# Optimization experiments

Hardware: AMD Instinct MI355X
Metric: run time of the kernel (lower is better)

The kernel has to match this reference:

```python
import jax, jax.numpy as jnp
import numpy as np

EPS_W = 1e-9


def area2d(a, b, c):
    # signed parallelogram area; a/b/c are [..., >=2] points
    return (b[..., 0] - a[..., 0]) * (c[..., 1] - a[..., 1]) - (b[..., 1] - a[..., 1]) * (c[..., 0] - a[..., 0])


def lookup_table(size):
    # square table of 2d points (x, y) in [-1, 1], matching torch meshgrid('ij') + rot90
    lin = jnp.linspace(-1.0, 1.0, size, dtype=jnp.float32)
    xx, yy = jnp.meshgrid(lin, lin, indexing='ij')
    t = jnp.stack([xx, yy], axis=-1)
    return jnp.rot90(t, 1, axes=(0, 1))  # [S,S,2]


def grid_sample_bilinear(img, grid):
    # img [C,H,W]; grid [...,2] with (x,y) in [-1,1]; bilinear, zero padding, align_corners=True
    C, H, W = img.shape
    x, y = grid[..., 0], grid[..., 1]
    ix = (x + 1.0) * (W - 1) * 0.5
    iy = (y + 1.0) * (H - 1) * 0.5
    ix0 = jnp.floor(ix)
    iy0 = jnp.floor(iy)
    ix1 = ix0 + 1.0
    iy1 = iy0 + 1.0
    wx1 = ix - ix0
    wx0 = 1.0 - wx1
    wy1 = iy - iy0
    wy0 = 1.0 - wy1

    def tap(iyf, ixf):
        inb = (ixf >= 0) & (ixf <= W - 1) & (iyf >= 0) & (iyf <= H - 1)
        ii = jnp.clip(ixf, 0, W - 1).astype(jnp.int32)
        jj = jnp.clip(iyf, 0, H - 1).astype(jnp.int32)
        return img[:, jj, ii] * inb.astype(img.dtype)  # [C, ...]

    return (tap(iy0, ix0) * (wy0 * wx0) + tap(iy0, ix1) * (wy0 * wx1)
            + tap(iy1, ix0) * (wy1 * wx0) + tap(iy1, ix1) * (wy1 * wx1))


def _render(vertices, uv, uvmap, faces, uvfaces, size):
    pts = lookup_table(size)              # [S,S,2]
    uvn = uv * 2.0 - 1.0                  # uv scaled to [-1,1] as in __init__
    tris = vertices[faces]                # [K,3,3]
    uvt = uvn[uvfaces]                    # [K,3,2]

    # backface cull mask (z-component of cross(v1-v0, v2-v0) > 0)
    e1 = tris[:, 1] - tris[:, 0]
    e2 = tris[:, 2] - tris[:, 0]
    normal_z = e1[:, 0] * e2[:, 1] - e1[:, 1] * e2[:, 0]
    valid = normal_z > 0

    zinit = jnp.min(vertices, axis=0)[-1]
    result0 = jnp.zeros((4, size, size), jnp.float32)
    zbuf0 = jnp.full((size, size), zinit, dtype=jnp.float32)

    def step(carry, xs):
        result, zbuf = carry
        tri, uvtri, ok = xs               # tri [3,3], uvtri [3,2], ok scalar bool
        tri2d = tri[:, :2]
        w = area2d(tri2d[0], tri2d[1], tri2d[2])
        # sub areas against every pixel (dense equivalent of AABB + inside masks)
        pAB = area2d(tri2d[1], pts, tri2d[0])   # [S,S]
        pCB = area2d(tri2d[2], pts, tri2d[1])
        pCA = area2d(tri2d[0], pts, tri2d[2])
        inside = (pAB > 0) & (pCB > 0) & (pCA > 0)
        ws = jnp.where(w >= EPS_W, w, 1.0)      # safe divide; masked out below
        w1 = pCB / ws
        w2 = pCA / ws
        w3 = 1.0 - w1 - w2
        z = w1 * tri[0, 2] + w2 * tri[1, 2] + w3 * tri[2, 2]   # [S,S]
        mask = ok & (w >= EPS_W) & inside & (z >= zbuf)
        # barycentric uv interpolation + bilinear texture lookup
        ptsUV = w1[..., None] * uvtri[0] + w2[..., None] * uvtri[1] + w3[..., None] * uvtri[2]  # [S,S,2]
        rgb = grid_sample_bilinear(uvmap, ptsUV)  # [3,S,S]
        zbuf = jnp.where(mask, z, zbuf)
        rgba = jnp.concatenate([rgb, jnp.ones((1, size, size), result.dtype)], axis=0)
        result = jnp.where(mask[None], rgba, result)
        return (result, zbuf), None

    (result, _), _ = jax.lax.scan(step, (result0, zbuf0), (tris, uvt, valid))
    return result


def setup_inputs() -> dict:
    key = jax.random.key(0)
    k0, k1, k2, k3, k4 = jax.random.split(key, 5)
    V, K, M, T, S = 1500, 1500, 2000, 1024, 512
    vertices = jax.random.normal(k0, (V, 3), dtype=jnp.float32)
    faces = jax.random.randint(k1, (K, 3), 0, V)
    uv = jax.random.uniform(k2, (M, 2), dtype=jnp.float32)
    uvfaces = jax.random.randint(k3, (K, 3), 0, M)
    uvmap = jax.random.normal(k4, (3, T, T), dtype=jnp.float32)
    return {"vertices": vertices, "faces": faces, "uv": uv,
            "uvfaces": uvfaces, "uvmap": uvmap, "size": S}


def reference(vertices, faces, uv, uvfaces, uvmap, size):
    return _render(vertices, uv, uvmap, faces, uvfaces, size)
```

## Files before the change

kernel.cpp:

```cpp
#include <hip/hip_runtime.h>
#include <hip/hip_fp16.h>
#include <cmath>

#pragma clang fp contract(off)

#define MAXK 2048

struct TriUV {
  float u0x, u0y, u1x, u1y;
  float u2x, u2y, pad0, pad1;
};

struct __align__(128) TriRec {
  uint4 ap;
  float4 mt;
  float4 q0;
  float4 q1;
  float4 q2;
  float4 q3;
  float4 pad0, pad1;
};

__device__ __forceinline__ float h2f(unsigned v) {
  __half_raw r; r.x = (unsigned short)v;
  return __half2float(__half(r));
}
__device__ __forceinline__ unsigned f2h(float v) {
  return (unsigned)__half_as_ushort(__float2half(v));
}
__device__ __forceinline__ unsigned pkh(float lo, float hi) {
  return f2h(lo) | (f2h(hi) << 16);
}
__device__ __forceinline__ unsigned fmapu(float f) {
  unsigned b = __float_as_uint(f);
  return (b & 0x80000000u) ? ~b : (b | 0x80000000u);
}
__device__ __forceinline__ float funmap(unsigned m) {
  return __uint_as_float((m & 0x80000000u) ? (m ^ 0x80000000u) : ~m);
}

__device__ __forceinline__ float lin_at(int i, int n) {
#pragma clang fp contract(off)
  if (i == n - 1) return 1.0f;
  float step = (float)i / (float)(n - 1);
  return (-1.0f) * (1.0f - step) + 1.0f * step;
}

__global__ __launch_bounds__(256) void prep_kernel(
    const float* __restrict__ verts, const int* __restrict__ faces,
    const float* __restrict__ uv, const int* __restrict__ uvfaces, int V, int K,
    TriRec* __restrict__ rec, float4* __restrict__ bboxS,
    float4* __restrict__ planeS, TriUV* __restrict__ tuv,
    float* __restrict__ zinit) {
#pragma clang fp contract(off)
  __shared__ float smz[256];
  int tid = (int)threadIdx.x;
  int bid = (int)blockIdx.x;
  if (bid == 0) {
    float m = 3.402823466e38f;
    for (int i = tid; i < V; i += 256) m = fminf(m, verts[3 * i + 2]);
    smz[tid] = m;
    __syncthreads();
    for (int s2 = 128; s2 > 0; s2 >>= 1) {
      if (tid < s2) smz[tid] = fminf(smz[tid], smz[tid + s2]);
      __syncthreads();
    }
    if (tid == 0) *zinit = smz[0];
    return;
  }
  int t = (bid - 1) * 256 + tid;
  if (t >= K) return;
  int i0 = faces[3 * t + 0], i1 = faces[3 * t + 1], i2 = faces[3 * t + 2];
  float t0x = verts[3 * i0 + 0], t0y = verts[3 * i0 + 1], z0 = verts[3 * i0 + 2];
  float t1x = verts[3 * i1 + 0], t1y = verts[3 * i1 + 1], z1 = verts[3 * i1 + 2];
  float t2x = verts[3 * i2 + 0], t2y = verts[3 * i2 + 1], z2 = verts[3 * i2 + 2];
  int j0 = uvfaces[3 * t + 0], j1 = uvfaces[3 * t + 1], j2 = uvfaces[3 * t + 2];
  TriUV u;
  u.u0x = uv[2 * j0 + 0] * 2.0f - 1.0f;
  u.u0y = uv[2 * j0 + 1] * 2.0f - 1.0f;
  u.u1x = uv[2 * j1 + 0] * 2.0f - 1.0f;
  u.u1y = uv[2 * j1 + 1] * 2.0f - 1.0f;
  u.u2x = uv[2 * j2 + 0] * 2.0f - 1.0f;
  u.u2y = uv[2 * j2 + 1] * 2.0f - 1.0f;
  u.pad0 = 0.0f; u.pad1 = 0.0f;
  tuv[t] = u;
  float w = (t1x - t0x) * (t2y - t0y) - (t1y - t0y) * (t2x - t0x);
  if (w < 1e-9f) {
    bboxS[t] = make_float4(3.0e38f, -3.0e38f, 3.0e38f, -3.0e38f);
    return;
  }
  float dAy = t0y - t1y, dAx = t0x - t1x;
  float dBy = t1y - t2y, dBx = t1x - t2x;
  float dCy = t2y - t0y, dCx = t2x - t0x;
  bboxS[t] = make_float4(fminf(fminf(t0x, t1x), t2x),
                         fmaxf(fmaxf(t0x, t1x), t2x),
                         fminf(fminf(t0y, t1y), t2y),
                         fmaxf(fmaxf(t0y, t1y), t2y));
  float fA = t1y * dAx - t1x * dAy;
  float fB = t2y * dBx - t2x * dBy;
  float fC = t0y * dCx - t0x * dCy;
  float sA = fabsf(dAy) + fabsf(dAx) + fabsf(fA);
  float sB = fabsf(dBy) + fabsf(dBx) + fabsf(fB);
  float sC = fabsf(dCy) + fabsf(dCx) + fabsf(fC);
  float M = fmaxf(fmaxf(sA, sB), sC) * 9.766e-4f + 1e-4f;
  TriRec r;
  r.ap = make_uint4(pkh(dAy, dAx), pkh(fA, dBy), pkh(dBx, fB), pkh(dCy, dCx));
  r.mt = make_float4(M, fC, __int_as_float(t), 0.0f);
  r.q0 = make_float4(t1x, t1y, dAy, dAx);
  r.q1 = make_float4(t2x, t2y, dBy, dBx);
  r.q2 = make_float4(t0x, t0y, dCy, dCx);
  r.q3 = make_float4(z0, z1, z2, w);
  r.pad0 = make_float4(0.f, 0.f, 0.f, 0.f);
  r.pad1 = make_float4(0.f, 0.f, 0.f, 0.f);
  rec[t] = r;
  float zmx = fmaxf(fmaxf(z0, z1), z2);
  float gatef = zmx + 1e-3f + 1e-4f / w;
  float gx = (z0 * dBy + z1 * dCy + z2 * dAy) / w;
  float gy = -(z0 * dBx + z1 * dCx + z2 * dAx) / w;
  float cc = (z0 * fB + z1 * fC + z2 * fA) / w;
  float mm = (fabsf(z0 * fB) + fabsf(z1 * fC) + fabsf(z2 * fA) +
              fabsf(z0 * dBy) + fabsf(z1 * dCy) + fabsf(z2 * dAy) +
              fabsf(z0 * dBx) + fabsf(z1 * dCx) + fabsf(z2 * dAx)) *
                 (2e-6f / w) +
             1e-3f + 1e-4f / w + 1e-4f;
  planeS[t] = make_float4(gx, gy, cc + mm, gatef);
}

__global__ __launch_bounds__(1024) void render_kernel(
    const TriRec* __restrict__ rec, const float4* __restrict__ bboxS,
    const float4* __restrict__ planeS, int N, const TriUV* __restrict__ tuv,
    const float* __restrict__ zinitp, const float* __restrict__ uvmap, int T,
    float* __restrict__ out, int S) {
#pragma clang fp contract(off)
  __shared__ uint4 s_g[MAXK];
  __shared__ unsigned long long s_key[256];
  __shared__ unsigned s_zu[256];
  __shared__ unsigned s_hist[256];
  __shared__ int s_cur[256];
  __shared__ unsigned s_wsum[4];

  int tid = (int)threadIdx.x;
  int wv = tid >> 6, ln = tid & 63;
  int s = wv >> 2, q = wv & 3;
  int pix = (q << 6) + ln;
  int tilesX = S >> 4;
  int tileX = (int)blockIdx.x % tilesX;
  int tileY = (int)blockIdx.x / tilesX;
  int j = (tileX << 4) + (pix & 15);
  int i = (tileY << 4) + (pix >> 4);
  float px = lin_at(j, S);
  float py = lin_at(S - 1 - i, S);
  float pxlo = lin_at(tileX << 4, S);
  float pxhi = lin_at((tileX << 4) + 15, S);
  float pylo = lin_at(S - 1 - ((tileY << 4) + 15), S);
  float pyhi = lin_at(S - 1 - (tileY << 4), S);

  float zinit = *zinitp;
  unsigned zinit_m = fmapu(zinit);
  if (tid < 256) {
    s_zu[tid] = zinit_m;
    s_key[tid] = ((unsigned long long)zinit_m << 32);
    s_hist[tid] = 0u;
  }
  volatile unsigned* vzu = s_zu;
  __syncthreads();

  bool kA = false, kB = false;
  int bA = 0, bB = 0;
  unsigned gA = 0, gB = 0;
  {
    int t = tid;
    if (t < N) {
      float4 bb = bboxS[t];
      if (bb.x <= pxhi && bb.y >= pxlo && bb.z <= pyhi && bb.w >= pylo) {
        float4 pl = planeS[t];
        float ub = pl.z + fmaxf(pl.x * pxlo, pl.x * pxhi) +
                   fmaxf(pl.y * pylo, pl.y * pyhi);
        float tg = fminf(pl.w, ub);
        kA = true;
        bA = min(max((int)((4.0f - tg) * 32.0f), 0), 255);
        gA = fmapu(tg);
      }
    }
    t = tid + 1024;
    if (t < N) {
      float4 bb = bboxS[t];
      if (bb.x <= pxhi && bb.y >= pxlo && bb.z <= pyhi && bb.w >= pylo) {
        float4 pl = planeS[t];
        float ub = pl.z + fmaxf(pl.x * pxlo, pl.x * pxhi) +
                   fmaxf(pl.y * pylo, pl.y * pyhi);
        float tg = fminf(pl.w, ub);
        kB = true;
        bB = min(max((int)((4.0f - tg) * 32.0f), 0), 255);
        gB = fmapu(tg);
      }
    }
  }
  if (kA) atomicAdd(&s_hist[bA], 1u);
  if (kB) atomicAdd(&s_hist[bB], 1u);
  __syncthreads();
  unsigned hx = 0, hinc = 0;
  if (tid < 256) {
    hx = s_hist[tid];
    unsigned v = hx;
#pragma unroll
    for (int d = 1; d < 64; d <<= 1) {
      unsigned tv = __shfl_up(v, d, 64);
      if (ln >= d) v += tv;
    }
    if (ln == 63) s_wsum[wv] = v;
    hinc = v;
  }
  __syncthreads();
  if (tid < 256) {
    unsigned add = 0;
    for (int w2 = 0; w2 < wv; ++w2) add += s_wsum[w2];
    hinc += add;
    s_hist[tid] = hinc;
    s_cur[tid] = (int)(hinc - hx);
  }
  __syncthreads();
  int nk = (int)s_hist[255];
  if (kA) {
    int sl = atomicAdd(&s_cur[bA], 1);
    float ef = (bA == 0) ? 3.402823466e38f : (4.0f - (float)bA * 0.03125f);
    s_g[sl] = make_uint4(fmapu(ef), gA, (unsigned)tid, 0u);
  }
  if (kB) {
    int sl = atomicAdd(&s_cur[bB], 1);
    float ef = (bB == 0) ? 3.402823466e38f : (4.0f - (float)bB * 0.03125f);
    s_g[sl] = make_uint4(fmapu(ef), gB, (unsigned)(tid + 1024), 0u);
  }
  __syncthreads();

  for (int a = s; a < nk; a += 4) {
    uint4 g = s_g[a];
    unsigned zb = vzu[pix];
    if (__all(g.x < zb)) break;
    if (g.y >= zb) {
      const TriRec* r = &rec[g.z];
      uint4 ap = r->ap;
      float4 mt = r->mt;
      float M = mt.x, fC = mt.y;
      float aA = fmaf(px, h2f(ap.x & 0xffffu),
                      fmaf(-py, h2f(ap.x >> 16), h2f(ap.y & 0xffffu)));
      float aB = fmaf(px, h2f(ap.y >> 16),
                      fmaf(-py, h2f(ap.z & 0xffffu), h2f(ap.z >> 16)));
      float aC = fmaf(px, h2f(ap.w & 0xffffu),
                      fmaf(-py, h2f(ap.w >> 16), fC));
      if (fminf(fminf(aA, aB), aC) > -M) {
        float4 q0 = r->q0, q1 = r->q1, q2 = r->q2;
        float pAB = (px - q0.x) * q0.z - (py - q0.y) * q0.w;
        float pCB = (px - q1.x) * q1.z - (py - q1.y) * q1.w;
        float pCA = (px - q2.x) * q2.z - (py - q2.y) * q2.w;
        if (pAB > 0.0f && pCB > 0.0f && pCA > 0.0f) {
          float4 q3 = r->q3;
          float w = q3.w;
          float bzf = funmap(vzu[pix]);
          float zs = (pCB * q3.x + pCA * q3.y) + ((w - pCB) - pCA) * q3.z;
          if (w < 1e-3f || zs >= (bzf - 1e-3f) * w) {
            float w1 = pCB / w;
            float w2 = pCA / w;
            float w3 = (1.0f - w1) - w2;
            float z = (w1 * q3.x + w2 * q3.y) + w3 * q3.z;
            int o = __float_as_int(mt.z);
            unsigned zm = fmapu(z);
            unsigned long long key =
                ((unsigned long long)zm << 32) | (unsigned)(o + 1);
            atomicMax(&s_key[pix], key);
            atomicMax(&s_zu[pix], zm);
          }
        }
      }
    }
  }
  __syncthreads();

  if (tid < 256) {
    unsigned long long key = s_key[tid];
    unsigned oP1 = (unsigned)(key & 0xFFFFFFFFULL);
    float o0 = 0.0f, o1 = 0.0f, o2 = 0.0f, o3 = 0.0f;
    if (oP1 != 0) {
      int o = (int)oP1 - 1;
      const TriRec* r = &rec[o];
      float4 q1 = r->q1, q2 = r->q2, q3 = r->q3;
      float pCB = (px - q1.x) * q1.z - (py - q1.y) * q1.w;
      float pCA = (px - q2.x) * q2.z - (py - q2.y) * q2.w;
      float w1 = pCB / q3.w;
      float w2 = pCA / q3.w;
      float w3 = (1.0f - w1) - w2;
      TriUV u = tuv[o];
      float x = (w1 * u.u0x + w2 * u.u1x) + w3 * u.u2x;
      float y = (w1 * u.u0y + w2 * u.u1y) + w3 * u.u2y;
      float WH = (float)(T - 1);
      float fx = ((x + 1.0f) * WH) * 0.5f;
      float fy = ((y + 1.0f) * WH) * 0.5f;
      float ix0 = floorf(fx), iy0 = floorf(fy);
      float ix1 = ix0 + 1.0f, iy1 = iy0 + 1.0f;
      float wx1 = fx - ix0, wx0 = 1.0f - wx1;
      float wy1 = fy - iy0, wy0 = 1.0f - wy1;
      float w00 = wy0 * wx0, w01 = wy0 * wx1;
      float w10 = wy1 * wx0, w11 = wy1 * wx1;
      bool bx0 = (ix0 >= 0.0f) && (ix0 <= WH);
      bool bx1 = (ix1 >= 0.0f) && (ix1 <= WH);
      bool by0 = (iy0 >= 0.0f) && (iy0 <= WH);
      bool by1 = (iy1 >= 0.0f) && (iy1 <= WH);
      float m00 = (by0 && bx0) ? 1.0f : 0.0f;
      float m01 = (by0 && bx1) ? 1.0f : 0.0f;
      float m10 = (by1 && bx0) ? 1.0f : 0.0f;
      float m11 = (by1 && bx1) ? 1.0f : 0.0f;
      int cx0 = (int)fminf(fmaxf(ix0, 0.0f), WH);
      int cx1 = (int)fminf(fmaxf(ix1, 0.0f), WH);
      int cy0 = (int)fminf(fmaxf(iy0, 0.0f), WH);
      int cy1 = (int)fminf(fmaxf(iy1, 0.0f), WH);
      int TT = T * T;
      int i00 = cy0 * T + cx0, i01 = cy0 * T + cx1;
      int i10 = cy1 * T + cx0, i11 = cy1 * T + cx1;
      {
        const float* img = uvmap;
        float v00 = img[i00] * m00, v01 = img[i01] * m01;
        float v10 = img[i10] * m10, v11 = img[i11] * m11;
        o0 = ((v00 * w00 + v01 * w01) + v10 * w10) + v11 * w11;
      }
      {
        const float* img = uvmap + TT;
        float v00 = img[i00] * m00, v01 = img[i01] * m01;
        float v10 = img[i10] * m10, v11 = img[i11] * m11;
        o1 = ((v00 * w00 + v01 * w01) + v10 * w10) + v11 * w11;
      }
      {
        const float* img = uvmap + 2 * TT;
        float v00 = img[i00] * m00, v01 = img[i01] * m01;
        float v10 = img[i10] * m10, v11 = img[i11] * m11;
        o2 = ((v00 * w00 + v01 * w01) + v10 * w10) + v11 * w11;
      }
      o3 = 1.0f;
    }
    int p = i * S + j;
    int SS = S * S;
    out[p] = o0;
    out[SS + p] = o1;
    out[2 * SS + p] = o2;
    out[3 * SS + p] = o3;
  }
}

extern "C" void kernel_launch(void* const* d_in, const int* in_sizes, int n_in,
                              void* d_out, int out_size, void* d_ws,
                              size_t ws_size, hipStream_t stream) {
  const float* verts = (const float*)d_in[0];
  const int* faces = (const int*)d_in[1];
  const float* uv = (const float*)d_in[2];
  const int* uvfaces = (const int*)d_in[3];
  const float* uvmap = (const float*)d_in[4];
  int V = in_sizes[0] / 3;
  int K = in_sizes[1] / 3;
  int T = (int)lroundf(sqrtf((float)(in_sizes[4] / 3)));
  int S = (int)lroundf(sqrtf((float)(out_size / 4)));
  float* outp = (float*)d_out;

  char* ws = (char*)d_ws;
  size_t off = 0;
  auto alloc = [&](size_t bytes) {
    void* p = ws + off;
    off = (off + bytes + 255) & ~(size_t)255;
    return p;
  };
  float* zinit = (float*)alloc(4);
  TriRec* rec = (TriRec*)alloc((size_t)MAXK * sizeof(TriRec));
  float4* bboxS = (float4*)alloc((size_t)MAXK * 16);
  float4* planeS = (float4*)alloc((size_t)MAXK * 16);
  TriUV* tuv = (TriUV*)alloc((size_t)K * sizeof(TriUV));

  int pblocks = 1 + (K + 255) / 256;
  prep_kernel<<<pblocks, 256, 0, stream>>>(verts, faces, uv, uvfaces, V, K,
                                           rec, bboxS, planeS, tuv, zinit);
  int tiles = (S >> 4) * (S >> 4);
  render_kernel<<<tiles, 1024, 0, stream>>>(rec, bboxS, planeS, K, tuv, zinit,
                                            uvmap, T, outp, S);
}
```

Before: 31.79 us.

## Pack candidate list into 32-bit keys with strided layout and batched early-exit

Replaces the 16-byte per-candidate record in shared memory with a single 32-bit word that holds a quantized gate depth and the triangle index. Entries are stored strided per wave-group so each group reads four candidates with one vector load. The early-termination test now runs once per batch of four, deriving the bucket bound from the quantized gate. The local depth bound is also updated from each thread's own writes. This cuts LDS footprint and load traffic. The risks are looser culling from quantization and coarser early exit, plus reliance on triangle indices fitting in 11 bits.

```diff
diff --git a/kernel.cpp b/kernel.cpp
--- a/kernel.cpp
+++ b/kernel.cpp
@@ -132,7 +132,7 @@
     const float* __restrict__ zinitp, const float* __restrict__ uvmap, int T,
     float* __restrict__ out, int S) {
 #pragma clang fp contract(off)
-  __shared__ uint4 s_g[MAXK];
+  __shared__ __align__(16) unsigned s_gq[MAXK];
   __shared__ unsigned long long s_key[256];
   __shared__ unsigned s_zu[256];
   __shared__ unsigned s_hist[256];
@@ -162,6 +162,8 @@
     s_key[tid] = ((unsigned long long)zinit_m << 32);
     s_hist[tid] = 0u;
   }
+  s_gq[tid] = 0u;
+  s_gq[tid + 1024] = 0u;
   volatile unsigned* vzu = s_zu;
   __syncthreads();
 
@@ -223,55 +225,75 @@
   int nk = (int)s_hist[255];
   if (kA) {
     int sl = atomicAdd(&s_cur[bA], 1);
-    float ef = (bA == 0) ? 3.402823466e38f : (4.0f - (float)bA * 0.03125f);
-    s_g[sl] = make_uint4(fmapu(ef), gA, (unsigned)tid, 0u);
+    unsigned tgq = (gA + 0x7FFu) & ~0x7FFu;
+    s_gq[(sl & 3) * 512 + (sl >> 2)] = tgq | (unsigned)tid;
   }
   if (kB) {
     int sl = atomicAdd(&s_cur[bB], 1);
-    float ef = (bB == 0) ? 3.402823466e38f : (4.0f - (float)bB * 0.03125f);
-    s_g[sl] = make_uint4(fmapu(ef), gB, (unsigned)(tid + 1024), 0u);
-  }
-  __syncthreads();
-
-  for (int a = s; a < nk; a += 4) {
-    uint4 g = s_g[a];
+    unsigned tgq = (gB + 0x7FFu) & ~0x7FFu;
+    s_gq[(sl & 3) * 512 + (sl >> 2)] = tgq | (unsigned)(tid + 1024);
+  }
+  __syncthreads();
+
+  {
+    int ecount = (nk > s) ? ((nk - 1 - s) >> 2) + 1 : 0;
+    const unsigned* gq = s_gq + (s << 9);
     unsigned zb = vzu[pix];
-    if (__all(g.x < zb)) break;
-    if (g.y >= zb) {
-      const TriRec* r = &rec[g.z];
-      uint4 ap = r->ap;
-      float4 mt = r->mt;
-      float M = mt.x, fC = mt.y;
-      float aA = fmaf(px, h2f(ap.x & 0xffffu),
-                      fmaf(-py, h2f(ap.x >> 16), h2f(ap.y & 0xffffu)));
-      float aB = fmaf(px, h2f(ap.y >> 16),
-                      fmaf(-py, h2f(ap.z & 0xffffu), h2f(ap.z >> 16)));
-      float aC = fmaf(px, h2f(ap.w & 0xffffu),
-                      fmaf(-py, h2f(ap.w >> 16), fC));
-      if (fminf(fminf(aA, aB), aC) > -M) {
-        float4 q0 = r->q0, q1 = r->q1, q2 = r->q2;
-        float pAB = (px - q0.x) * q0.z - (py - q0.y) * q0.w;
-        float pCB = (px - q1.x) * q1.z - (py - q1.y) * q1.w;
-        float pCA = (px - q2.x) * q2.z - (py - q2.y) * q2.w;
-        if (pAB > 0.0f && pCB > 0.0f && pCA > 0.0f) {
-          float4 q3 = r->q3;
-          float w = q3.w;
-          float bzf = funmap(vzu[pix]);
-          float zs = (pCB * q3.x + pCA * q3.y) + ((w - pCB) - pCA) * q3.z;
-          if (w < 1e-3f || zs >= (bzf - 1e-3f) * w) {
-            float w1 = pCB / w;
-            float w2 = pCA / w;
-            float w3 = (1.0f - w1) - w2;
-            float z = (w1 * q3.x + w2 * q3.y) + w3 * q3.z;
-            int o = __float_as_int(mt.z);
-            unsigned zm = fmapu(z);
-            unsigned long long key =
-                ((unsigned long long)zm << 32) | (unsigned)(o + 1);
-            atomicMax(&s_key[pix], key);
-            atomicMax(&s_zu[pix], zm);
+    for (int e4 = 0; e4 < ecount; e4 += 4) {
+      uint4 G = *(const uint4*)(gq + e4);
+      {
+        unsigned zf = vzu[pix];
+        zb = max(zb, zf);
+      }
+#pragma unroll
+      for (int k = 0; k < 4; ++k) {
+        unsigned gk = (k == 0) ? G.x : (k == 1) ? G.y : (k == 2) ? G.z : G.w;
+        if ((gk & ~0x7FFu) >= zb) {
+          int idx = (int)(gk & 0x7FFu);
+          const TriRec* r = &rec[idx];
+          uint4 ap = r->ap;
+          float4 mt = r->mt;
+          float M = mt.x, fC = mt.y;
+          float aA = fmaf(px, h2f(ap.x & 0xffffu),
+                          fmaf(-py, h2f(ap.x >> 16), h2f(ap.y & 0xffffu)));
+          float aB = fmaf(px, h2f(ap.y >> 16),
+                          fmaf(-py, h2f(ap.z & 0xffffu), h2f(ap.z >> 16)));
+          float aC = fmaf(px, h2f(ap.w & 0xffffu),
+                          fmaf(-py, h2f(ap.w >> 16), fC));
+          if (fminf(fminf(aA, aB), aC) > -M) {
+            float4 q0 = r->q0, q1 = r->q1, q2 = r->q2;
+            float pAB = (px - q0.x) * q0.z - (py - q0.y) * q0.w;
+            float pCB = (px - q1.x) * q1.z - (py - q1.y) * q1.w;
+            float pCA = (px - q2.x) * q2.z - (py - q2.y) * q2.w;
+            if (pAB > 0.0f && pCB > 0.0f && pCA > 0.0f) {
+              float4 q3 = r->q3;
+              float w = q3.w;
+              float bzf = funmap(vzu[pix]);
+              float zs = (pCB * q3.x + pCA * q3.y) + ((w - pCB) - pCA) * q3.z;
+              if (w < 1e-3f || zs >= (bzf - 1e-3f) * w) {
+                float w1 = pCB / w;
+                float w2 = pCA / w;
+                float w3 = (1.0f - w1) - w2;
+                float z = (w1 * q3.x + w2 * q3.y) + w3 * q3.z;
+                unsigned zm = fmapu(z);
+                unsigned long long key =
+                    ((unsigned long long)zm << 32) | (unsigned)(idx + 1);
+                atomicMax(&s_key[pix], key);
+                atomicMax(&s_zu[pix], zm);
+                zb = max(zb, zm);
+              }
+            }
           }
         }
       }
+      int vi = min(e4 + 3, ecount - 1) - e4;
+      unsigned gv = (vi == 0) ? G.x : (vi == 1) ? G.y : (vi == 2) ? G.z : G.w;
+      float efu = funmap(gv & ~0x7FFu);
+      int b2 = (int)((4.0f - efu) * 32.0f);
+      b2 = min(max(b2, 0), 255);
+      unsigned em = (b2 == 0) ? 0xFFFFFFFFu
+                              : fmapu(4.0f - (float)b2 * 0.03125f);
+      if (__all(em < zb)) break;
     }
   }
   __syncthreads();
```

Result: slower. 33.97 us (+6.9%).

## Compact culled triangles in prep and drop separate shared z buffer

Applied to the files above, without the earlier changes.

The prep kernel now gives each non-culled triangle a dense slot through an atomic counter and records a triangle-to-slot map. The render kernel then scans only the surviving triangles instead of all K. The separate shared z array and its atomicMax are removed; the depth is read from the high word of the packed 64-bit key instead. The cost is an extra memset launch to reset the counter, an indirection through slotOf in the shading pass, and a slot order that changes from run to run.

```diff
diff --git a/kernel.cpp b/kernel.cpp
--- a/kernel.cpp
+++ b/kernel.cpp
@@ -50,8 +50,9 @@
     const float* __restrict__ verts, const int* __restrict__ faces,
     const float* __restrict__ uv, const int* __restrict__ uvfaces, int V, int K,
     TriRec* __restrict__ rec, float4* __restrict__ bboxS,
-    float4* __restrict__ planeS, TriUV* __restrict__ tuv,
-    float* __restrict__ zinit) {
+    float4* __restrict__ planeS, int* __restrict__ slotOf,
+    TriUV* __restrict__ tuv, float* __restrict__ zinit,
+    int* __restrict__ counter) {
 #pragma clang fp contract(off)
   __shared__ float smz[256];
   int tid = (int)threadIdx.x;
@@ -85,17 +86,16 @@
   u.pad0 = 0.0f; u.pad1 = 0.0f;
   tuv[t] = u;
   float w = (t1x - t0x) * (t2y - t0y) - (t1y - t0y) * (t2x - t0x);
-  if (w < 1e-9f) {
-    bboxS[t] = make_float4(3.0e38f, -3.0e38f, 3.0e38f, -3.0e38f);
-    return;
-  }
+  if (w < 1e-9f) return;
+  int slot = atomicAdd(counter, 1);
+  slotOf[t] = slot;
   float dAy = t0y - t1y, dAx = t0x - t1x;
   float dBy = t1y - t2y, dBx = t1x - t2x;
   float dCy = t2y - t0y, dCx = t2x - t0x;
-  bboxS[t] = make_float4(fminf(fminf(t0x, t1x), t2x),
-                         fmaxf(fmaxf(t0x, t1x), t2x),
-                         fminf(fminf(t0y, t1y), t2y),
-                         fmaxf(fmaxf(t0y, t1y), t2y));
+  bboxS[slot] = make_float4(fminf(fminf(t0x, t1x), t2x),
+                            fmaxf(fmaxf(t0x, t1x), t2x),
+                            fminf(fminf(t0y, t1y), t2y),
+                            fmaxf(fmaxf(t0y, t1y), t2y));
   float fA = t1y * dAx - t1x * dAy;
   float fB = t2y * dBx - t2x * dBy;
   float fC = t0y * dCx - t0x * dCy;
@@ -112,7 +112,7 @@
   r.q3 = make_float4(z0, z1, z2, w);
   r.pad0 = make_float4(0.f, 0.f, 0.f, 0.f);
   r.pad1 = make_float4(0.f, 0.f, 0.f, 0.f);
-  rec[t] = r;
+  rec[slot] = r;
   float zmx = fmaxf(fmaxf(z0, z1), z2);
   float gatef = zmx + 1e-3f + 1e-4f / w;
   float gx = (z0 * dBy + z1 * dCy + z2 * dAy) / w;
@@ -123,18 +123,18 @@
               fabsf(z0 * dBx) + fabsf(z1 * dCx) + fabsf(z2 * dAx)) *
                  (2e-6f / w) +
              1e-3f + 1e-4f / w + 1e-4f;
-  planeS[t] = make_float4(gx, gy, cc + mm, gatef);
+  planeS[slot] = make_float4(gx, gy, cc + mm, gatef);
 }
 
 __global__ __launch_bounds__(1024) void render_kernel(
     const TriRec* __restrict__ rec, const float4* __restrict__ bboxS,
-    const float4* __restrict__ planeS, int N, const TriUV* __restrict__ tuv,
+    const float4* __restrict__ planeS, const int* __restrict__ countp,
+    const int* __restrict__ slotOf, const TriUV* __restrict__ tuv,
     const float* __restrict__ zinitp, const float* __restrict__ uvmap, int T,
     float* __restrict__ out, int S) {
 #pragma clang fp contract(off)
   __shared__ uint4 s_g[MAXK];
   __shared__ unsigned long long s_key[256];
-  __shared__ unsigned s_zu[256];
   __shared__ unsigned s_hist[256];
   __shared__ int s_cur[256];
   __shared__ unsigned s_wsum[4];
@@ -155,14 +155,14 @@
   float pylo = lin_at(S - 1 - ((tileY << 4) + 15), S);
   float pyhi = lin_at(S - 1 - (tileY << 4), S);
 
+  int N = *countp;
   float zinit = *zinitp;
   unsigned zinit_m = fmapu(zinit);
   if (tid < 256) {
-    s_zu[tid] = zinit_m;
     s_key[tid] = ((unsigned long long)zinit_m << 32);
     s_hist[tid] = 0u;
   }
-  volatile unsigned* vzu = s_zu;
+  volatile unsigned* vhk = (volatile unsigned*)s_key;
   __syncthreads();
 
   bool kA = false, kB = false;
@@ -235,7 +235,7 @@
 
   for (int a = s; a < nk; a += 4) {
     uint4 g = s_g[a];
-    unsigned zb = vzu[pix];
+    unsigned zb = vhk[(pix << 1) + 1];
     if (__all(g.x < zb)) break;
     if (g.y >= zb) {
       const TriRec* r = &rec[g.z];
@@ -256,7 +256,7 @@
         if (pAB > 0.0f && pCB > 0.0f && pCA > 0.0f) {
           float4 q3 = r->q3;
           float w = q3.w;
-          float bzf = funmap(vzu[pix]);
+          float bzf = funmap(zb);
           float zs = (pCB * q3.x + pCA * q3.y) + ((w - pCB) - pCA) * q3.z;
           if (w < 1e-3f || zs >= (bzf - 1e-3f) * w) {
             float w1 = pCB / w;
@@ -268,7 +268,6 @@
             unsigned long long key =
                 ((unsigned long long)zm << 32) | (unsigned)(o + 1);
             atomicMax(&s_key[pix], key);
-            atomicMax(&s_zu[pix], zm);
           }
         }
       }
@@ -282,7 +281,8 @@
     float o0 = 0.0f, o1 = 0.0f, o2 = 0.0f, o3 = 0.0f;
     if (oP1 != 0) {
       int o = (int)oP1 - 1;
-      const TriRec* r = &rec[o];
+      int slot = slotOf[o];
+      const TriRec* r = &rec[slot];
       float4 q1 = r->q1, q2 = r->q2, q3 = r->q3;
       float pCB = (px - q1.x) * q1.z - (py - q1.y) * q1.w;
       float pCA = (px - q2.x) * q2.z - (py - q2.y) * q2.w;
@@ -367,15 +367,20 @@
     return p;
   };
   float* zinit = (float*)alloc(4);
+  int* counter = (int*)alloc(4);
   TriRec* rec = (TriRec*)alloc((size_t)MAXK * sizeof(TriRec));
   float4* bboxS = (float4*)alloc((size_t)MAXK * 16);
   float4* planeS = (float4*)alloc((size_t)MAXK * 16);
+  int* slotOf = (int*)alloc((size_t)K * 4);
   TriUV* tuv = (TriUV*)alloc((size_t)K * sizeof(TriUV));
 
+  hipMemsetAsync(counter, 0, 4, stream);
   int pblocks = 1 + (K + 255) / 256;
   prep_kernel<<<pblocks, 256, 0, stream>>>(verts, faces, uv, uvfaces, V, K,
-                                           rec, bboxS, planeS, tuv, zinit);
+                                           rec, bboxS, planeS, slotOf, tuv,
+                                           zinit, counter);
   int tiles = (S >> 4) * (S >> 4);
-  render_kernel<<<tiles, 1024, 0, stream>>>(rec, bboxS, planeS, K, tuv, zinit,
-                                            uvmap, T, outp, S);
-}
+  render_kernel<<<tiles, 1024, 0, stream>>>(rec, bboxS, planeS, counter,
+                                            slotOf, tuv, zinit, uvmap, T,
+                                            outp, S);
+}
```

Result: slower. 34.24 us (+7.7%).
